# Kernel optimization log

Hardware: AMD Instinct MI355X
Metric: run time of the kernel (lower is better)

Reference implementation:

```python
import jax, jax.numpy as jnp
import numpy as np

NUM_HEADS = 16
HIDDEN = 1024
DIM = HIDDEN // NUM_HEADS  # 64
NEG = -1e8
LN_EPS = 1e-5


def setup_inputs() -> dict:
    key = jax.random.key(0)
    ks = jax.random.split(key, 8)
    B, Lq, Lk = 8, 512, 2048
    s = 0.02
    return {
        "input_embed": jax.random.normal(ks[0], (B, Lq, HIDDEN), jnp.float32),
        "kg_embed": jax.random.normal(ks[1], (B, Lk, HIDDEN), jnp.float32),
        "input_mask": jnp.ones((B, Lq), jnp.float32),
        "kg_mask": jnp.ones((B, Lk), jnp.float32),
        "Wq": jax.random.normal(ks[2], (DIM, DIM), jnp.float32) * s,
        "Wk": jax.random.normal(ks[3], (DIM, DIM), jnp.float32) * s,
        "Wv": jax.random.normal(ks[4], (DIM, DIM), jnp.float32) * s,
        "W_lin": jax.random.normal(ks[5], (HIDDEN, HIDDEN), jnp.float32) * s,
        "b_lin": jnp.zeros((HIDDEN,), jnp.float32),
        "ln_gamma": jnp.ones((HIDDEN,), jnp.float32),
        "ln_beta": jnp.zeros((HIDDEN,), jnp.float32),
    }


def reference(input_embed, kg_embed, input_mask, kg_mask, Wq, Wk, Wv, W_lin, b_lin, ln_gamma, ln_beta):
    B, Lq, H = input_embed.shape
    Lk = kg_embed.shape[1]
    # split heads: per-head slices share the SAME dim x dim q/k/v weights
    xq = input_embed.reshape(B, Lq, NUM_HEADS, DIM)
    xk = kg_embed.reshape(B, Lk, NUM_HEADS, DIM)
    q = jnp.einsum('bqhd,ed->bqhe', xq, Wq)  # Linear: x @ W.T
    k = jnp.einsum('bkhd,ed->bkhe', xk, Wk)
    v = jnp.einsum('bkhd,ed->bkhe', xk, Wv)
    scores = jnp.einsum('bqhd,bkhd->bhqk', q, k) / np.sqrt(DIM)  # [B,H,Lq,Lk]
    # additive masks: query-side and key-side
    scores = scores + ((1.0 - input_mask) * NEG)[:, None, :, None] \
                    + ((1.0 - kg_mask) * NEG)[:, None, None, :]
    attn = jax.nn.softmax(scores, axis=-1)
    ctx = jnp.einsum('bhqk,bkhd->bqhd', attn, v).reshape(B, Lq, H)  # concat heads
    lin = ctx @ W_lin.T + b_lin
    x = jax.nn.gelu(lin, approximate=False) + input_embed  # nn.GELU() is exact erf
    mu = jnp.mean(x, axis=-1, keepdims=True)
    var = jnp.mean(jnp.square(x - mu), axis=-1, keepdims=True)
    return (x - mu) * jax.lax.rsqrt(var + LN_EPS) * ln_gamma + ln_beta
```

## Files before the change

kernel.cpp:

```cpp
#include <hip/hip_runtime.h>
#include <cstdint>

#define BATCH 8
#define LQ 512
#define LK 2048
#define NH 16
#define DIM 64
#define HID 1024
#define NTOK (BATCH * LQ)
#define NKT (LK / 64)
#define SC 0.1803368801111204f
#define NEGM (-1.4426950408889634e8f)

typedef _Float16 f16x8 __attribute__((ext_vector_type(8)));
typedef __fp16 half2v __attribute__((ext_vector_type(2)));
typedef float f32x4 __attribute__((ext_vector_type(4)));

#define MFMA(a, b, c) __builtin_amdgcn_mfma_f32_16x16x32_f16((a), (b), (c), 0, 0, 0)

__device__ __forceinline__ f16x8 ld8(const _Float16* p) { return *(const f16x8*)p; }

__device__ __forceinline__ void gl_lds16(const void* g, void* l) {
  __builtin_amdgcn_global_load_lds(
      (const __attribute__((address_space(1))) uint32_t*)g,
      (__attribute__((address_space(3))) uint32_t*)l, 16, 0, 0);
}

__device__ __forceinline__ void lds_barrier() {
  asm volatile("s_waitcnt lgkmcnt(0)" ::: "memory");
  __builtin_amdgcn_s_barrier();
}

__device__ __forceinline__ f16x8 cvt8(const float* p) {
  const float4 a = *(const float4*)p;
  const float4 b = *(const float4*)(p + 4);
  f16x8 v;
  v[0] = (_Float16)a.x; v[1] = (_Float16)a.y; v[2] = (_Float16)a.z; v[3] = (_Float16)a.w;
  v[4] = (_Float16)b.x; v[5] = (_Float16)b.y; v[6] = (_Float16)b.z; v[7] = (_Float16)b.w;
  return v;
}

__device__ __forceinline__ uint2 pk4(float a, float b, float c, float d) {
  union { half2v h2[2]; uint2 u; } t;
  t.h2[0] = __builtin_amdgcn_cvt_pkrtz(a, b);
  t.h2[1] = __builtin_amdgcn_cvt_pkrtz(c, d);
  return t.u;
}

__device__ __forceinline__ f16x8 pk8(float4 a, float4 b) {
  union { half2v h2[4]; f16x8 v; } t;
  t.h2[0] = __builtin_amdgcn_cvt_pkrtz(a.x, a.y);
  t.h2[1] = __builtin_amdgcn_cvt_pkrtz(a.z, a.w);
  t.h2[2] = __builtin_amdgcn_cvt_pkrtz(b.x, b.y);
  t.h2[3] = __builtin_amdgcn_cvt_pkrtz(b.z, b.w);
  return t.v;
}

__global__ __launch_bounds__(512, 2) void attn_kernel(
    const float* __restrict__ Xq, const float* __restrict__ Xk,
    const float* __restrict__ Wq, const float* __restrict__ Wk,
    const float* __restrict__ Wv, const float* __restrict__ kg_mask,
    _Float16* __restrict__ ctx) {
  __shared__ __align__(16) _Float16 Kl[2][64 * 72];
  __shared__ __align__(16) _Float16 Vl[2][64 * 72];
  __shared__ __align__(16) _Float16 Pl[8][2][16 * 72];
  __shared__ __align__(16) float    Ml[LK];
  const int tid = threadIdx.x;
  const int wave = tid >> 6, lane = tid & 63, l16 = lane & 15, quad = lane >> 4;
  const int kw = wave & 3;
  const int b = blockIdx.x >> 4, h = blockIdx.x & 15;
  const int qbase = blockIdx.y * 256;
  const float* Xg = Xk + (size_t)b * LK * HID + h * 64;
  const float* mg = kg_mask + (size_t)b * LK;

  const float* xrow0 = Xg + (size_t)(kw * 16 + l16) * HID + quad * 8;
  float4 xf0, xf1, xf2, xf3;
  auto loadX = [&](int kt) {
    const float* xr = xrow0 + (size_t)kt * HID;
    xf0 = *(const float4*)(xr);
    xf1 = *(const float4*)(xr + 4);
    xf2 = *(const float4*)(xr + 32);
    xf3 = *(const float4*)(xr + 36);
  };
  loadX(0);

  {
    const float4 m4 = *(const float4*)(mg + tid * 4);
    float4 mo;
    mo.x = (1.f - m4.x) * NEGM;
    mo.y = (1.f - m4.y) * NEGM;
    mo.z = (1.f - m4.z) * NEGM;
    mo.w = (1.f - m4.w) * NEGM;
    *(float4*)(Ml + tid * 4) = mo;
  }

  f16x8 aq0[2], aq1[2];
  {
    f16x8 wq0[4], wq1[4];
#pragma unroll
    for (int nt = 0; nt < 4; ++nt) {
      const float* wp = Wq + (nt * 16 + l16) * DIM + quad * 8;
      wq0[nt] = cvt8(wp);
      wq1[nt] = cvt8(wp + 32);
    }
#pragma unroll
    for (int qt = 0; qt < 2; ++qt) {
      const int qg = qbase + wave * 32 + qt * 16 + l16;
      const float* xpq = Xq + (size_t)(b * LQ + qg) * HID + h * 64 + quad * 8;
      const f16x8 bq0 = cvt8(xpq), bq1 = cvt8(xpq + 32);
#pragma unroll
      for (int nt = 0; nt < 4; ++nt) {
        f32x4 d = {0.f, 0.f, 0.f, 0.f};
        d = MFMA(wq0[nt], bq0, d);
        d = MFMA(wq1[nt], bq1, d);
        *(uint2*)&Pl[wave][qt][l16 * 72 + nt * 16 + quad * 4] =
            pk4(d[0] * SC, d[1] * SC, d[2] * SC, d[3] * SC);
      }
      aq0[qt] = ld8(&Pl[wave][qt][l16 * 72 + quad * 8]);
      aq1[qt] = ld8(&Pl[wave][qt][l16 * 72 + 32 + quad * 8]);
    }
  }

  const float* Wsel = (wave < 4) ? Wk : Wv;
  f16x8 aw0[4], aw1[4];
#pragma unroll
  for (int nt = 0; nt < 4; ++nt) {
    const float* wp = Wsel + (nt * 16 + l16) * DIM + quad * 8;
    aw0[nt] = cvt8(wp);
    aw1[nt] = cvt8(wp + 32);
  }

  const f32x4 z4 = {0.f, 0.f, 0.f, 0.f};

  {
    const f16x8 bx0 = pk8(xf0, xf1), bx1 = pk8(xf2, xf3);
    if (wave < 4) {
#pragma unroll
      for (int nt = 0; nt < 4; ++nt) {
        f32x4 d = z4;
        d = MFMA(aw0[nt], bx0, d);
        d = MFMA(aw1[nt], bx1, d);
        *(uint2*)&Kl[0][(kw * 16 + l16) * 72 + nt * 16 + quad * 4] =
            pk4(d[0], d[1], d[2], d[3]);
      }
    } else {
#pragma unroll
      for (int dt = 0; dt < 4; ++dt) {
        f32x4 d = z4;
        d = MFMA(bx0, aw0[dt], d);
        d = MFMA(bx1, aw1[dt], d);
        *(uint2*)&Vl[0][(dt * 16 + l16) * 72 + kw * 16 + quad * 4] =
            pk4(d[0], d[1], d[2], d[3]);
      }
    }
  }
  loadX(64);
  lds_barrier();

  f32x4 o[2][4];
  float l_run[2] = {0.f, 0.f};
#pragma unroll
  for (int qt = 0; qt < 2; ++qt)
#pragma unroll
    for (int i = 0; i < 4; ++i) o[qt][i] = z4;

  for (int t = 0; t < NKT; ++t) {
    const int buf = t & 1;
    const int kt = t * 64;

    if (t + 1 < NKT) {
      const f16x8 bx0 = pk8(xf0, xf1), bx1 = pk8(xf2, xf3);
      if (wave < 4) {
#pragma unroll
        for (int nt = 0; nt < 4; ++nt) {
          f32x4 d = z4;
          d = MFMA(aw0[nt], bx0, d);
          d = MFMA(aw1[nt], bx1, d);
          *(uint2*)&Kl[buf ^ 1][(kw * 16 + l16) * 72 + nt * 16 + quad * 4] =
              pk4(d[0], d[1], d[2], d[3]);
        }
      } else {
#pragma unroll
        for (int dt = 0; dt < 4; ++dt) {
          f32x4 d = z4;
          d = MFMA(bx0, aw0[dt], d);
          d = MFMA(bx1, aw1[dt], d);
          *(uint2*)&Vl[buf ^ 1][(dt * 16 + l16) * 72 + kw * 16 + quad * 4] =
              pk4(d[0], d[1], d[2], d[3]);
        }
      }
      if (t + 2 < NKT) loadX(kt + 128);
    }

    float4 mv[4];
#pragma unroll
    for (int nt = 0; nt < 4; ++nt)
      mv[nt] = *(const float4*)(Ml + kt + nt * 16 + quad * 4);

    float p[2][4][4];
    __builtin_amdgcn_s_setprio(1);
#pragma unroll
    for (int nt = 0; nt < 4; ++nt) {
      const f16x8 kb0 = ld8(&Kl[buf][(nt * 16 + l16) * 72 + quad * 8]);
      const f16x8 kb1 = ld8(&Kl[buf][(nt * 16 + l16) * 72 + 32 + quad * 8]);
#pragma unroll
      for (int qt = 0; qt < 2; ++qt) {
        f32x4 s = z4;
        s = MFMA(kb0, aq0[qt], s);
        s = MFMA(kb1, aq1[qt], s);
        const float e0 = __builtin_amdgcn_exp2f(s[0] + mv[nt].x);
        const float e1 = __builtin_amdgcn_exp2f(s[1] + mv[nt].y);
        const float e2 = __builtin_amdgcn_exp2f(s[2] + mv[nt].z);
        const float e3 = __builtin_amdgcn_exp2f(s[3] + mv[nt].w);
        l_run[qt] += (e0 + e1) + (e2 + e3);
        p[qt][nt][0] = e0; p[qt][nt][1] = e1; p[qt][nt][2] = e2; p[qt][nt][3] = e3;
      }
    }
    __builtin_amdgcn_s_setprio(0);

#pragma unroll
    for (int qt = 0; qt < 2; ++qt)
#pragma unroll
      for (int nt = 0; nt < 4; ++nt)
        *(uint2*)&Pl[wave][qt][l16 * 72 + nt * 16 + quad * 4] =
            pk4(p[qt][nt][0], p[qt][nt][1], p[qt][nt][2], p[qt][nt][3]);
    f16x8 ap0[2], ap1[2];
#pragma unroll
    for (int qt = 0; qt < 2; ++qt) {
      ap0[qt] = ld8(&Pl[wave][qt][l16 * 72 + quad * 8]);
      ap1[qt] = ld8(&Pl[wave][qt][l16 * 72 + 32 + quad * 8]);
    }

    __builtin_amdgcn_s_setprio(1);
#pragma unroll
    for (int dt = 0; dt < 4; ++dt) {
      const f16x8 vb0 = ld8(&Vl[buf][(dt * 16 + l16) * 72 + quad * 8]);
      const f16x8 vb1 = ld8(&Vl[buf][(dt * 16 + l16) * 72 + 32 + quad * 8]);
#pragma unroll
      for (int qt = 0; qt < 2; ++qt) {
        o[qt][dt] = MFMA(vb0, ap0[qt], o[qt][dt]);
        o[qt][dt] = MFMA(vb1, ap1[qt], o[qt][dt]);
      }
    }
    __builtin_amdgcn_s_setprio(0);

    lds_barrier();
  }

  float inv[2];
#pragma unroll
  for (int qt = 0; qt < 2; ++qt) {
    float s = l_run[qt];
    s += __shfl_xor(s, 16);
    s += __shfl_xor(s, 32);
    inv[qt] = 1.f / s;
  }
#pragma unroll
  for (int qt = 0; qt < 2; ++qt) {
    const int qg = qbase + wave * 32 + qt * 16 + l16;
    _Float16* base = ctx + (size_t)(b * LQ + qg) * HID + h * 64;
#pragma unroll
    for (int dt = 0; dt < 4; ++dt)
      *(uint2*)(base + dt * 16 + quad * 4) =
          pk4(o[qt][dt][0] * inv[qt], o[qt][dt][1] * inv[qt],
              o[qt][dt][2] * inv[qt], o[qt][dt][3] * inv[qt]);
  }
}

__global__ __launch_bounds__(256) void wconv_kernel(const float* __restrict__ W,
                                                    _Float16* __restrict__ Wh) {
  const int i = blockIdx.x * 256 + threadIdx.x;
  const float4 v = ((const float4*)W)[i];
  ((uint2*)Wh)[i] = pk4(v.x, v.y, v.z, v.w);
}

__global__ __launch_bounds__(512) void linear_kernel(const _Float16* __restrict__ A,
                                                     const _Float16* __restrict__ Wh,
                                                     const float* __restrict__ bias,
                                                     const float* __restrict__ resid,
                                                     float* __restrict__ Xout) {
  __shared__ __align__(16) _Float16 Al[2][128 * 64];
  __shared__ __align__(16) _Float16 Bl[2][128 * 64];
  const int tid = threadIdx.x;
  const int wave = tid >> 6, lane = tid & 63, l16 = lane & 15, quad = lane >> 4;
  const int wm = wave >> 2, wn = wave & 3;
  const int nbase = blockIdx.x * 128, mbase = blockIdx.y * 128;
  const int srow = wave * 16 + (lane >> 3);
  const int sc = lane & 7;

  auto stage = [&](int kk, int nbuf) {
#pragma unroll
    for (int i = 0; i < 2; ++i) {
      const int row = srow + i * 8;
      const int c = sc ^ (row & 7);
      gl_lds16(A + (size_t)(mbase + row) * HID + kk + c * 8,
               &Al[nbuf][(wave * 16 + i * 8) * 64]);
      gl_lds16(Wh + (size_t)(nbase + row) * HID + kk + c * 8,
               &Bl[nbuf][(wave * 16 + i * 8) * 64]);
    }
  };

  const f32x4 z4 = {0.f, 0.f, 0.f, 0.f};
  f32x4 acc[4][2];
#pragma unroll
  for (int mt = 0; mt < 4; ++mt)
#pragma unroll
    for (int nt = 0; nt < 2; ++nt) acc[mt][nt] = z4;

  stage(0, 0);
  for (int t = 0; t < HID / 64; ++t) {
    const int buf = t & 1;
    __syncthreads();
    if (t + 1 < HID / 64) stage((t + 1) * 64, buf ^ 1);
    const int sw = l16 & 7;
    f16x8 b0[2], b1[2];
#pragma unroll
    for (int nt = 0; nt < 2; ++nt) {
      const int brow = wn * 32 + nt * 16 + l16;
      b0[nt] = ld8(&Bl[buf][brow * 64 + (quad ^ sw) * 8]);
      b1[nt] = ld8(&Bl[buf][brow * 64 + ((quad + 4) ^ sw) * 8]);
    }
#pragma unroll
    for (int mt = 0; mt < 4; ++mt) {
      const int arow = wm * 64 + mt * 16 + l16;
      const f16x8 a0 = ld8(&Al[buf][arow * 64 + (quad ^ sw) * 8]);
      const f16x8 a1 = ld8(&Al[buf][arow * 64 + ((quad + 4) ^ sw) * 8]);
#pragma unroll
      for (int nt = 0; nt < 2; ++nt) {
        acc[mt][nt] = MFMA(a0, b0[nt], acc[mt][nt]);
        acc[mt][nt] = MFMA(a1, b1[nt], acc[mt][nt]);
      }
    }
  }
#pragma unroll
  for (int nt = 0; nt < 2; ++nt) {
    const int col = nbase + wn * 32 + nt * 16 + l16;
    const float bv = bias[col];
#pragma unroll
    for (int mt = 0; mt < 4; ++mt) {
#pragma unroll
      for (int r = 0; r < 4; ++r) {
        const int row = mbase + wm * 64 + mt * 16 + quad * 4 + r;
        const float v = acc[mt][nt][r] + bv;
        const float g = 0.5f * v * (1.f + erff(v * 0.70710678118654752f));
        Xout[(size_t)row * HID + col] = g + resid[(size_t)row * HID + col];
      }
    }
  }
}

__global__ __launch_bounds__(256) void ln_kernel(const float* __restrict__ X,
                                                 const float* __restrict__ gamma,
                                                 const float* __restrict__ beta,
                                                 float* __restrict__ out) {
  const int row = blockIdx.x, tid = threadIdx.x;
  const int lane = tid & 63, wave = tid >> 6;
  const float4 v = *(const float4*)(X + (size_t)row * HID + tid * 4);
  float s1 = v.x + v.y + v.z + v.w;
  float s2 = v.x * v.x + v.y * v.y + v.z * v.z + v.w * v.w;
#pragma unroll
  for (int off = 1; off < 64; off <<= 1) {
    s1 += __shfl_xor(s1, off);
    s2 += __shfl_xor(s2, off);
  }
  __shared__ float r1[4], r2[4];
  if (lane == 0) { r1[wave] = s1; r2[wave] = s2; }
  __syncthreads();
  s1 = r1[0] + r1[1] + r1[2] + r1[3];
  s2 = r2[0] + r2[1] + r2[2] + r2[3];
  const float mu = s1 * (1.f / HID);
  const float var = s2 * (1.f / HID) - mu * mu;
  const float rstd = rsqrtf(var + 1e-5f);
  const float4 g = *(const float4*)(gamma + tid * 4);
  const float4 be = *(const float4*)(beta + tid * 4);
  float4 ov;
  ov.x = (v.x - mu) * rstd * g.x + be.x;
  ov.y = (v.y - mu) * rstd * g.y + be.y;
  ov.z = (v.z - mu) * rstd * g.z + be.z;
  ov.w = (v.w - mu) * rstd * g.w + be.w;
  *(float4*)(out + (size_t)row * HID + tid * 4) = ov;
}

extern "C" void kernel_launch(void* const* d_in, const int* in_sizes, int n_in,
                              void* d_out, int out_size, void* d_ws, size_t ws_size,
                              hipStream_t stream) {
  (void)in_sizes; (void)n_in; (void)out_size; (void)ws_size;
  const float* input_embed = (const float*)d_in[0];
  const float* kg_embed    = (const float*)d_in[1];
  const float* kg_mask = (const float*)d_in[3];
  const float* Wq    = (const float*)d_in[4];
  const float* Wk    = (const float*)d_in[5];
  const float* Wv    = (const float*)d_in[6];
  const float* W_lin = (const float*)d_in[7];
  const float* b_lin = (const float*)d_in[8];
  const float* gamma = (const float*)d_in[9];
  const float* beta  = (const float*)d_in[10];

  char* ws = (char*)d_ws;
  _Float16* ctx = (_Float16*)(ws);
  float*    Xb  = (float*)(ws + (8u << 20));
  _Float16* Wh  = (_Float16*)(ws + (24u << 20));

  attn_kernel<<<dim3(128, 2), dim3(512), 0, stream>>>(input_embed, kg_embed, Wq, Wk, Wv,
                                                      kg_mask, ctx);
  wconv_kernel<<<dim3(1024), dim3(256), 0, stream>>>(W_lin, Wh);
  linear_kernel<<<dim3(8, 32), dim3(512), 0, stream>>>(ctx, Wh, b_lin, input_embed, Xb);
  ln_kernel<<<dim3(NTOK), dim3(256), 0, stream>>>(Xb, gamma, beta, (float*)d_out);
}
```

Before: 213.8 us.

## Halve per-wave query tiles to double attention grid and occupancy, pad LDS rows

Each wave now handles one 16-row query tile instead of two, so the attention grid doubles to 128x4 blocks of 128 queries and launch bounds ask for 4 blocks per CU. LDS row stride changes from 72 to 76 halves and the P buffer shrinks to a single tile per wave. The aim is to fill the 256 CUs better and hide latency with more resident waves, at the cost of recomputing the K/V projection twice as often per (batch, head) and halving MFMA reuse of each loaded K/V fragment.

```diff
diff --git a/kernel.cpp b/kernel.cpp
--- a/kernel.cpp
+++ b/kernel.cpp
@@ -9,6 +9,7 @@
 #define HID 1024
 #define NTOK (BATCH * LQ)
 #define NKT (LK / 64)
+#define KP 76
 #define SC 0.1803368801111204f
 #define NEGM (-1.4426950408889634e8f)
 
@@ -56,20 +57,20 @@
   return t.v;
 }
 
-__global__ __launch_bounds__(512, 2) void attn_kernel(
+__global__ __launch_bounds__(512, 4) void attn_kernel(
     const float* __restrict__ Xq, const float* __restrict__ Xk,
     const float* __restrict__ Wq, const float* __restrict__ Wk,
     const float* __restrict__ Wv, const float* __restrict__ kg_mask,
     _Float16* __restrict__ ctx) {
-  __shared__ __align__(16) _Float16 Kl[2][64 * 72];
-  __shared__ __align__(16) _Float16 Vl[2][64 * 72];
-  __shared__ __align__(16) _Float16 Pl[8][2][16 * 72];
+  __shared__ __align__(16) _Float16 Kl[2][64 * KP];
+  __shared__ __align__(16) _Float16 Vl[2][64 * KP];
+  __shared__ __align__(16) _Float16 Pl[8][16 * KP];
   __shared__ __align__(16) float    Ml[LK];
   const int tid = threadIdx.x;
   const int wave = tid >> 6, lane = tid & 63, l16 = lane & 15, quad = lane >> 4;
   const int kw = wave & 3;
   const int b = blockIdx.x >> 4, h = blockIdx.x & 15;
-  const int qbase = blockIdx.y * 256;
+  const int qbase = blockIdx.y * 128;
   const float* Xg = Xk + (size_t)b * LK * HID + h * 64;
   const float* mg = kg_mask + (size_t)b * LK;
 
@@ -94,7 +95,7 @@
     *(float4*)(Ml + tid * 4) = mo;
   }
 
-  f16x8 aq0[2], aq1[2];
+  f16x8 aq0, aq1;
   {
     f16x8 wq0[4], wq1[4];
 #pragma unroll
@@ -103,22 +104,19 @@
       wq0[nt] = cvt8(wp);
       wq1[nt] = cvt8(wp + 32);
     }
-#pragma unroll
-    for (int qt = 0; qt < 2; ++qt) {
-      const int qg = qbase + wave * 32 + qt * 16 + l16;
-      const float* xpq = Xq + (size_t)(b * LQ + qg) * HID + h * 64 + quad * 8;
-      const f16x8 bq0 = cvt8(xpq), bq1 = cvt8(xpq + 32);
-#pragma unroll
-      for (int nt = 0; nt < 4; ++nt) {
-        f32x4 d = {0.f, 0.f, 0.f, 0.f};
-        d = MFMA(wq0[nt], bq0, d);
-        d = MFMA(wq1[nt], bq1, d);
-        *(uint2*)&Pl[wave][qt][l16 * 72 + nt * 16 + quad * 4] =
-            pk4(d[0] * SC, d[1] * SC, d[2] * SC, d[3] * SC);
-      }
-      aq0[qt] = ld8(&Pl[wave][qt][l16 * 72 + quad * 8]);
-      aq1[qt] = ld8(&Pl[wave][qt][l16 * 72 + 32 + quad * 8]);
-    }
+    const int qg = qbase + wave * 16 + l16;
+    const float* xpq = Xq + (size_t)(b * LQ + qg) * HID + h * 64 + quad * 8;
+    const f16x8 bq0 = cvt8(xpq), bq1 = cvt8(xpq + 32);
+#pragma unroll
+    for (int nt = 0; nt < 4; ++nt) {
+      f32x4 d = {0.f, 0.f, 0.f, 0.f};
+      d = MFMA(wq0[nt], bq0, d);
+      d = MFMA(wq1[nt], bq1, d);
+      *(uint2*)&Pl[wave][l16 * KP + nt * 16 + quad * 4] =
+          pk4(d[0] * SC, d[1] * SC, d[2] * SC, d[3] * SC);
+    }
+    aq0 = ld8(&Pl[wave][l16 * KP + quad * 8]);
+    aq1 = ld8(&Pl[wave][l16 * KP + 32 + quad * 8]);
   }
 
   const float* Wsel = (wave < 4) ? Wk : Wv;
@@ -140,7 +138,7 @@
         f32x4 d = z4;
         d = MFMA(aw0[nt], bx0, d);
         d = MFMA(aw1[nt], bx1, d);
-        *(uint2*)&Kl[0][(kw * 16 + l16) * 72 + nt * 16 + quad * 4] =
+        *(uint2*)&Kl[0][(kw * 16 + l16) * KP + nt * 16 + quad * 4] =
             pk4(d[0], d[1], d[2], d[3]);
       }
     } else {
@@ -149,7 +147,7 @@
         f32x4 d = z4;
         d = MFMA(bx0, aw0[dt], d);
         d = MFMA(bx1, aw1[dt], d);
-        *(uint2*)&Vl[0][(dt * 16 + l16) * 72 + kw * 16 + quad * 4] =
+        *(uint2*)&Vl[0][(dt * 16 + l16) * KP + kw * 16 + quad * 4] =
             pk4(d[0], d[1], d[2], d[3]);
       }
     }
@@ -157,12 +155,10 @@
   loadX(64);
   lds_barrier();
 
-  f32x4 o[2][4];
-  float l_run[2] = {0.f, 0.f};
-#pragma unroll
-  for (int qt = 0; qt < 2; ++qt)
-#pragma unroll
-    for (int i = 0; i < 4; ++i) o[qt][i] = z4;
+  f32x4 o[4];
+  float l_run = 0.f;
+#pragma unroll
+  for (int i = 0; i < 4; ++i) o[i] = z4;
 
   for (int t = 0; t < NKT; ++t) {
     const int buf = t & 1;
@@ -176,7 +172,7 @@
           f32x4 d = z4;
           d = MFMA(aw0[nt], bx0, d);
           d = MFMA(aw1[nt], bx1, d);
-          *(uint2*)&Kl[buf ^ 1][(kw * 16 + l16) * 72 + nt * 16 + quad * 4] =
+          *(uint2*)&Kl[buf ^ 1][(kw * 16 + l16) * KP + nt * 16 + quad * 4] =
               pk4(d[0], d[1], d[2], d[3]);
         }
       } else {
@@ -185,7 +181,7 @@
           f32x4 d = z4;
           d = MFMA(bx0, aw0[dt], d);
           d = MFMA(bx1, aw1[dt], d);
-          *(uint2*)&Vl[buf ^ 1][(dt * 16 + l16) * 72 + kw * 16 + quad * 4] =
+          *(uint2*)&Vl[buf ^ 1][(dt * 16 + l16) * KP + kw * 16 + quad * 4] =
               pk4(d[0], d[1], d[2], d[3]);
         }
       }
@@ -197,73 +193,55 @@
     for (int nt = 0; nt < 4; ++nt)
       mv[nt] = *(const float4*)(Ml + kt + nt * 16 + quad * 4);
 
-    float p[2][4][4];
+    float p[4][4];
     __builtin_amdgcn_s_setprio(1);
 #pragma unroll
     for (int nt = 0; nt < 4; ++nt) {
-      const f16x8 kb0 = ld8(&Kl[buf][(nt * 16 + l16) * 72 + quad * 8]);
-      const f16x8 kb1 = ld8(&Kl[buf][(nt * 16 + l16) * 72 + 32 + quad * 8]);
-#pragma unroll
-      for (int qt = 0; qt < 2; ++qt) {
-        f32x4 s = z4;
-        s = MFMA(kb0, aq0[qt], s);
-        s = MFMA(kb1, aq1[qt], s);
-        const float e0 = __builtin_amdgcn_exp2f(s[0] + mv[nt].x);
-        const float e1 = __builtin_amdgcn_exp2f(s[1] + mv[nt].y);
-        const float e2 = __builtin_amdgcn_exp2f(s[2] + mv[nt].z);
-        const float e3 = __builtin_amdgcn_exp2f(s[3] + mv[nt].w);
-        l_run[qt] += (e0 + e1) + (e2 + e3);
-        p[qt][nt][0] = e0; p[qt][nt][1] = e1; p[qt][nt][2] = e2; p[qt][nt][3] = e3;
-      }
+      const f16x8 kb0 = ld8(&Kl[buf][(nt * 16 + l16) * KP + quad * 8]);
+      const f16x8 kb1 = ld8(&Kl[buf][(nt * 16 + l16) * KP + 32 + quad * 8]);
+      f32x4 s = z4;
+      s = MFMA(kb0, aq0, s);
+      s = MFMA(kb1, aq1, s);
+      const float e0 = __builtin_amdgcn_exp2f(s[0] + mv[nt].x);
+      const float e1 = __builtin_amdgcn_exp2f(s[1] + mv[nt].y);
+      const float e2 = __builtin_amdgcn_exp2f(s[2] + mv[nt].z);
+      const float e3 = __builtin_amdgcn_exp2f(s[3] + mv[nt].w);
+      l_run += (e0 + e1) + (e2 + e3);
+      p[nt][0] = e0; p[nt][1] = e1; p[nt][2] = e2; p[nt][3] = e3;
     }
     __builtin_amdgcn_s_setprio(0);
 
 #pragma unroll
-    for (int qt = 0; qt < 2; ++qt)
-#pragma unroll
-      for (int nt = 0; nt < 4; ++nt)
-        *(uint2*)&Pl[wave][qt][l16 * 72 + nt * 16 + quad * 4] =
-            pk4(p[qt][nt][0], p[qt][nt][1], p[qt][nt][2], p[qt][nt][3]);
-    f16x8 ap0[2], ap1[2];
-#pragma unroll
-    for (int qt = 0; qt < 2; ++qt) {
-      ap0[qt] = ld8(&Pl[wave][qt][l16 * 72 + quad * 8]);
-      ap1[qt] = ld8(&Pl[wave][qt][l16 * 72 + 32 + quad * 8]);
-    }
+    for (int nt = 0; nt < 4; ++nt)
+      *(uint2*)&Pl[wave][l16 * KP + nt * 16 + quad * 4] =
+          pk4(p[nt][0], p[nt][1], p[nt][2], p[nt][3]);
+    const f16x8 ap0 = ld8(&Pl[wave][l16 * KP + quad * 8]);
+    const f16x8 ap1 = ld8(&Pl[wave][l16 * KP + 32 + quad * 8]);
 
     __builtin_amdgcn_s_setprio(1);
 #pragma unroll
     for (int dt = 0; dt < 4; ++dt) {
-      const f16x8 vb0 = ld8(&Vl[buf][(dt * 16 + l16) * 72 + quad * 8]);
-      const f16x8 vb1 = ld8(&Vl[buf][(dt * 16 + l16) * 72 + 32 + quad * 8]);
-#pragma unroll
-      for (int qt = 0; qt < 2; ++qt) {
-        o[qt][dt] = MFMA(vb0, ap0[qt], o[qt][dt]);
-        o[qt][dt] = MFMA(vb1, ap1[qt], o[qt][dt]);
-      }
+      const f16x8 vb0 = ld8(&Vl[buf][(dt * 16 + l16) * KP + quad * 8]);
+      const f16x8 vb1 = ld8(&Vl[buf][(dt * 16 + l16) * KP + 32 + quad * 8]);
+      o[dt] = MFMA(vb0, ap0, o[dt]);
+      o[dt] = MFMA(vb1, ap1, o[dt]);
     }
     __builtin_amdgcn_s_setprio(0);
 
     lds_barrier();
   }
 
-  float inv[2];
-#pragma unroll
-  for (int qt = 0; qt < 2; ++qt) {
-    float s = l_run[qt];
-    s += __shfl_xor(s, 16);
-    s += __shfl_xor(s, 32);
-    inv[qt] = 1.f / s;
-  }
-#pragma unroll
-  for (int qt = 0; qt < 2; ++qt) {
-    const int qg = qbase + wave * 32 + qt * 16 + l16;
+  float s = l_run;
+  s += __shfl_xor(s, 16);
+  s += __shfl_xor(s, 32);
+  const float inv = 1.f / s;
+  {
+    const int qg = qbase + wave * 16 + l16;
     _Float16* base = ctx + (size_t)(b * LQ + qg) * HID + h * 64;
 #pragma unroll
     for (int dt = 0; dt < 4; ++dt)
       *(uint2*)(base + dt * 16 + quad * 4) =
-          pk4(o[qt][dt][0] * inv[qt], o[qt][dt][1] * inv[qt],
-              o[qt][dt][2] * inv[qt], o[qt][dt][3] * inv[qt]);
+          pk4(o[dt][0] * inv, o[dt][1] * inv, o[dt][2] * inv, o[dt][3] * inv);
   }
 }
 
@@ -401,7 +379,7 @@
   float*    Xb  = (float*)(ws + (8u << 20));
   _Float16* Wh  = (_Float16*)(ws + (24u << 20));
 
-  attn_kernel<<<dim3(128, 2), dim3(512), 0, stream>>>(input_embed, kg_embed, Wq, Wk, Wv,
+  attn_kernel<<<dim3(128, 4), dim3(512), 0, stream>>>(input_embed, kg_embed, Wq, Wk, Wv,
                                                       kg_mask, ctx);
   wconv_kernel<<<dim3(1024), dim3(256), 0, stream>>>(W_lin, Wh);
   linear_kernel<<<dim3(8, 32), dim3(512), 0, stream>>>(ctx, Wh, b_lin, input_embed, Xb);
```

New measurement: 430.8 us. 101% more time.
